# Performance work log

Measured on AMD Instinct MI355X. Metric: run time of the kernel, lower is better.

## Reference

```python
import jax, jax.numpy as jnp
import numpy as np

B, T, DIN, H = 8, 512, 256, 512
D = 2 * H            # d_model = 1024
HEADS, DH, DEPTH, M = 8, 128, 2, 256  # M = nb_features
FF = 4 * D
KEPS = 1e-4          # performer kernel epsilon


def setup_inputs() -> dict:
    key = jax.random.key(0)
    ks = iter(jax.random.split(key, 64))
    def nrm(shape, s=1.0):
        return jax.random.normal(next(ks), shape, jnp.float32) * s
    inp = {"x": nrm((B, T, DIN))}
    # BiLSTM params, stacked over direction [2, ...]; torch gate order i,f,g,o
    for l, din in ((0, DIN), (1, D)):
        s = 1.0 / np.sqrt(H)
        inp[f"l{l}_Wih"] = nrm((2, 4 * H, din), s)
        inp[f"l{l}_Whh"] = nrm((2, 4 * H, H), s)
        inp[f"l{l}_bih"] = nrm((2, 4 * H), s)
        inp[f"l{l}_bhh"] = nrm((2, 4 * H), s)
    # FAVOR+ random projection (buffer), [nb_features, dim_head]
    inp["proj"] = nrm((M, DH))
    sd = 1.0 / np.sqrt(D)
    inp["ln1_g"] = jnp.ones((DEPTH, D)); inp["ln1_b"] = jnp.zeros((DEPTH, D))
    for n in ("Wq", "Wk", "Wv", "Wo"):
        inp[n] = nrm((DEPTH, D, D), sd)
    for n in ("bq", "bk", "bv", "bo"):
        inp[n] = jnp.zeros((DEPTH, D))
    inp["ln2_g"] = jnp.ones((DEPTH, D)); inp["ln2_b"] = jnp.zeros((DEPTH, D))
    inp["Wf1"] = nrm((DEPTH, D, FF), sd); inp["bf1"] = jnp.zeros((DEPTH, FF))
    inp["Wf2"] = nrm((DEPTH, FF, D), 1.0 / np.sqrt(FF)); inp["bf2"] = jnp.zeros((DEPTH, D))
    inp["cW1"] = nrm((D, H), sd); inp["cb1"] = jnp.zeros((H,))
    inp["cW2"] = nrm((H, 2), 1.0 / np.sqrt(H)); inp["cb2"] = jnp.zeros((2,))
    return inp


def _lstm_dir(x, Wih, Whh, bih, bhh, reverse):
    xs = jnp.swapaxes(x, 0, 1)                      # [T,B,Din]
    h0 = jnp.zeros((x.shape[0], H), x.dtype)
    def step(carry, xt):
        h, c = carry
        z = xt @ Wih.T + h @ Whh.T + bih + bhh      # [B,4H]
        i, f, g, o = jnp.split(z, 4, axis=-1)
        c = jax.nn.sigmoid(f) * c + jax.nn.sigmoid(i) * jnp.tanh(g)
        h = jax.nn.sigmoid(o) * jnp.tanh(c)
        return (h, c), h
    _, hs = jax.lax.scan(step, (h0, h0), xs, reverse=reverse)
    return jnp.swapaxes(hs, 0, 1)                   # [B,T,H], time-aligned


def _bilstm(x, Wih, Whh, bih, bhh):
    fwd = _lstm_dir(x, Wih[0], Whh[0], bih[0], bhh[0], False)
    bwd = _lstm_dir(x, Wih[1], Whh[1], bih[1], bhh[1], True)
    return jnp.concatenate([fwd, bwd], axis=-1)     # [B,T,2H]


def _ln(x, g, b):
    mu = jnp.mean(x, -1, keepdims=True)
    v = jnp.mean((x - mu) ** 2, -1, keepdims=True)
    return (x - mu) * jax.lax.rsqrt(v + 1e-5) * g + b


def _favor(data, proj, is_query):
    # softmax_kernel of performer-pytorch (eval mode, fixed projection)
    dn = DH ** -0.25
    dd = jnp.einsum('bhnd,md->bhnm', data * dn, proj)
    diag = jnp.sum(data * data, -1) * (dn * dn * 0.5)      # [b,h,n]
    if is_query:
        mx = jnp.max(dd, axis=-1, keepdims=True)
    else:
        mx = jnp.max(dd, axis=(-1, -2), keepdims=True)
    return (jnp.exp(dd - diag[..., None] - mx) + KEPS) * (M ** -0.5)


def _heads(x, W, b):
    return (x @ W + b).reshape(B, T, HEADS, DH).transpose(0, 2, 1, 3)


def reference(x, l0_Wih, l0_Whh, l0_bih, l0_bhh, l1_Wih, l1_Whh, l1_bih, l1_bhh,
              proj, ln1_g, ln1_b, Wq, bq, Wk, bk, Wv, bv, Wo, bo,
              ln2_g, ln2_b, Wf1, bf1, Wf2, bf2, cW1, cb1, cW2, cb2):
    h = _bilstm(x, l0_Wih, l0_Whh, l0_bih, l0_bhh)
    h = _bilstm(h, l1_Wih, l1_Whh, l1_bih, l1_bhh)          # [B,T,D]
    for i in range(DEPTH):
        # pre-norm FAVOR+ self-attention, non-causal linear attention
        y = _ln(h, ln1_g[i], ln1_b[i])
        q = _favor(_heads(y, Wq[i], bq[i]), proj, True)     # [b,h,n,m]
        k = _favor(_heads(y, Wk[i], bk[i]), proj, False)
        v = _heads(y, Wv[i], bv[i])                         # [b,h,n,d]
        dinv = 1.0 / jnp.einsum('bhnm,bhm->bhn', q, k.sum(axis=2))
        ctx = jnp.einsum('bhnm,bhnd->bhmd', k, v)
        o = jnp.einsum('bhnm,bhmd->bhnd', q, ctx) * dinv[..., None]
        o = o.transpose(0, 2, 1, 3).reshape(B, T, D)
        h = h + (o @ Wo[i] + bo[i])
        # pre-norm feedforward (GELU, mult 4)
        y = _ln(h, ln2_g[i], ln2_b[i])
        h = h + (jax.nn.gelu(y @ Wf1[i] + bf1[i], approximate=False) @ Wf2[i] + bf2[i])
    pooled = h.mean(axis=1)                                 # [B,D]
    logits = jax.nn.relu(pooled @ cW1 + cb1) @ cW2 + cb2    # [B,2]
    return logits
```

## Files before the change

### kernel.cpp

```cpp
#include <hip/hip_runtime.h>

#define KEPS 1e-4f

typedef __attribute__((ext_vector_type(8))) short bf16x8;
typedef __attribute__((ext_vector_type(4))) float f32x4;
typedef __attribute__((ext_vector_type(4))) unsigned u32x4;
typedef unsigned short u16;

__device__ float g_z0[2u*512*2048*8];
__device__ float g_z1[2u*512*2048*8];
__device__ float g_hres[8u*512*1024];
__device__ float g_qlin[8u*8*512*128];
__device__ float g_klin[8u*8*512*128];
__device__ float g_vlin[8u*8*512*128];
__device__ float g_qp[8u*8*512*256];
__device__ float g_ddb[8u*8*512*256];
__device__ float g_kT[8u*8*256*512];
__device__ float g_ctx[64u*256*128];
__device__ float g_bs0[2*2048];
__device__ float g_bs1[2*2048];
__device__ float g_diagq[32768];
__device__ float g_diagk[32768];
__device__ float g_kmx[64];
__device__ float g_ksum[64*256];
__device__ float g_dinv[32768];
__device__ __align__(16) unsigned g_hbuf[2*2*8*256];
__device__ float g_pooled[8*1024];

__device__ u16 g_xbf[8u*512*256];
__device__ u16 g_x1bf[8u*512*1024];
__device__ u16 g_ybf[8u*512*1024];
__device__ u16 g_ylo[8u*512*1024];
__device__ u16 g_obufbf[8u*512*1024];
__device__ u16 g_ffbbf[8u*512*4096];
__device__ u16 g_qhi[8u*8*512*128];
__device__ u16 g_qlo2[8u*8*512*128];
__device__ u16 g_khi[8u*8*512*128];
__device__ u16 g_klo2[8u*8*512*128];
__device__ u16 g_wih0b[2u*2048*256];
__device__ u16 g_wih1b[2u*2048*1024];
__device__ u16 g_wvt[2u*1024*1024];
__device__ u16 g_wot[2u*1024*1024];
__device__ u16 g_wf1t[2u*4096*1024];
__device__ u16 g_wf2t[2u*1024*4096];
__device__ u16 g_wqth[2u*1024*1024];
__device__ u16 g_wqtl[2u*1024*1024];
__device__ u16 g_wkth[2u*1024*1024];
__device__ u16 g_wktl[2u*1024*1024];
__device__ u16 g_projh[256*128];
__device__ u16 g_projl[256*128];

__device__ __forceinline__ float gelu_f(float x) {
  return 0.5f * x * (1.f + erff(x * 0.70710678118654752f));
}
__device__ __forceinline__ unsigned f2bf(float f) {
  unsigned x = __float_as_uint(f);
  return (x + 0x7FFFu + ((x >> 16) & 1u)) >> 16;
}
__device__ __forceinline__ float bf2f(unsigned h) {
  return __uint_as_float(h << 16);
}
__device__ __forceinline__ u32x4 ld16_sc1(const unsigned* p) {
  u32x4 v;
  asm volatile("global_load_dwordx4 %0, %1, off sc1\n\ts_waitcnt vmcnt(0)"
               : "=v"(v) : "v"(p) : "memory");
  return v;
}
__device__ __forceinline__ void st16_sc1(unsigned* p, u32x4 v) {
  asm volatile("global_store_dwordx4 %0, %1, off sc1" :: "v"(p), "v"(v) : "memory");
}
__device__ __forceinline__ void bar_raw() {
  asm volatile("s_waitcnt lgkmcnt(0)" ::: "memory");
  __builtin_amdgcn_sched_barrier(0);
  __builtin_amdgcn_s_barrier();
  __builtin_amdgcn_sched_barrier(0);
}
__device__ __forceinline__ void gll16(const void* g, void* l) {
  __builtin_amdgcn_global_load_lds(
      (const __attribute__((address_space(1))) void*)g,
      (__attribute__((address_space(3))) void*)l, 16, 0, 0);
}

__global__ void k_add2(float* __restrict__ dst, const float* __restrict__ a,
                       const float* __restrict__ b, int n) {
  int i = blockIdx.x * 256 + threadIdx.x;
  if (i < n) dst[i] = a[i] + b[i];
}
__global__ void k_cvt(const float* __restrict__ src, u16* __restrict__ dst, int n4) {
  int i = blockIdx.x * 256 + threadIdx.x;
  if (i < n4) {
    float4 v = ((const float4*)src)[i];
    ushort4 o; o.x=(u16)f2bf(v.x); o.y=(u16)f2bf(v.y); o.z=(u16)f2bf(v.z); o.w=(u16)f2bf(v.w);
    ((ushort4*)dst)[i] = o;
  }
}
__global__ void k_scale_split(const float* __restrict__ a, u16* __restrict__ dh,
                              u16* __restrict__ dl, float s, int n) {
  int i = blockIdx.x*256 + threadIdx.x;
  if (i < n) {
    float v = a[i]*s;
    unsigned h = f2bf(v);
    dh[i] = (u16)h; dl[i] = (u16)f2bf(v - bf2f(h));
  }
}
__global__ void k_w2bfT(const float* __restrict__ src, u16* __restrict__ dst,
                        int K, int N, long long sBS, long long dBS)
{
  __shared__ float tile[32][33];
  const int z = blockIdx.z;
  const int n0 = blockIdx.x*32, k0 = blockIdx.y*32;
  const int tx = threadIdx.x, ty = threadIdx.y;
  const float* s = src + (long long)z*sBS;
  u16* d = dst + (long long)z*dBS;
  #pragma unroll
  for (int j = 0; j < 4; ++j)
    tile[ty + j*8][tx] = s[(long long)(k0 + ty + j*8)*N + n0 + tx];
  __syncthreads();
  #pragma unroll
  for (int j = 0; j < 4; ++j)
    d[(long long)(n0 + ty + j*8)*K + k0 + tx] = (u16)f2bf(tile[tx][ty + j*8]);
}
__global__ void k_w2bfT_split(const float* __restrict__ src, u16* __restrict__ dh,
                              u16* __restrict__ dl, int K, int N,
                              long long sBS, long long dBS)
{
  __shared__ float tile[32][33];
  const int z = blockIdx.z;
  const int n0 = blockIdx.x*32, k0 = blockIdx.y*32;
  const int tx = threadIdx.x, ty = threadIdx.y;
  const float* s = src + (long long)z*sBS;
  #pragma unroll
  for (int j = 0; j < 4; ++j)
    tile[ty + j*8][tx] = s[(long long)(k0 + ty + j*8)*N + n0 + tx];
  __syncthreads();
  #pragma unroll
  for (int j = 0; j < 4; ++j) {
    const float v = tile[tx][ty + j*8];
    const unsigned h = f2bf(v);
    const long long off = (long long)z*dBS + (long long)(n0 + ty + j*8)*K + k0 + tx;
    dh[off] = (u16)h; dl[off] = (u16)f2bf(v - bf2f(h));
  }
}

template<int MODE>
__global__ __launch_bounds__(256)
void k_bgemm(const u16* __restrict__ A, const u16* __restrict__ Bw,
             const float* __restrict__ bias, void* __restrict__ Cv,
             int Ndim, int Kdim,
             long long aBS, long long bBS, long long cBS, long long biasBS)
{
  __shared__ __align__(16) u16 As[128*32];
  __shared__ __align__(16) u16 Bs[128*32];
  const int tid = threadIdx.x;
  const int m0 = blockIdx.y * 128, n0 = blockIdx.x * 128, z = blockIdx.z;
  const u16* Ab = A + (long long)z*aBS;
  const u16* Bb = Bw + (long long)z*bBS;
  const int wv = tid >> 6, l = tid & 63;
  const int wm = wv >> 1, wn = wv & 1;
  const int lr = l & 15, lk = l >> 4;
  const int lrow = l >> 2, lkq = (l & 3)*8;
  f32x4 acc[4][4];
  #pragma unroll
  for (int i=0;i<4;++i)
    #pragma unroll
    for (int j=0;j<4;++j) acc[i][j] = (f32x4){0.f,0.f,0.f,0.f};

  for (int k0 = 0; k0 < Kdim; k0 += 32) {
    #pragma unroll
    for (int q = 0; q < 2; ++q) {
      const int r = wv*32 + q*16 + lrow;
      gll16(&Ab[(long long)(m0 + r)*Kdim + k0 + lkq], &As[(wv*32 + q*16)*32]);
      gll16(&Bb[(long long)(n0 + r)*Kdim + k0 + lkq], &Bs[(wv*32 + q*16)*32]);
    }
    __syncthreads();
    bf16x8 af[4], bfr[4];
    #pragma unroll
    for (int i=0;i<4;++i) af[i]  = *(bf16x8*)&As[(wm*64 + i*16 + lr)*32 + lk*8];
    #pragma unroll
    for (int j=0;j<4;++j) bfr[j] = *(bf16x8*)&Bs[(wn*64 + j*16 + lr)*32 + lk*8];
    #pragma unroll
    for (int i=0;i<4;++i)
      #pragma unroll
      for (int j=0;j<4;++j)
        acc[i][j] = __builtin_amdgcn_mfma_f32_16x16x32_bf16(af[i], bfr[j], acc[i][j], 0, 0, 0);
    __syncthreads();
  }

  #pragma unroll
  for (int j=0;j<4;++j) {
    const int n = n0 + wn*64 + j*16 + lr;
    const float bvv = bias ? bias[(long long)z*biasBS + n] : 0.f;
    #pragma unroll
    for (int i=0;i<4;++i) {
      #pragma unroll
      for (int r=0;r<4;++r) {
        const int m = m0 + wm*64 + i*16 + lk*4 + r;
        float v = acc[i][j][r] + bvv;
        if (MODE == 0) {
          ((float*)Cv)[(long long)z*cBS + (long long)m*Ndim + n] = v;
        } else if (MODE == 1) {
          const int b_ = m >> 9, t_ = m & 511;
          ((float*)Cv)[(long long)z*cBS + ((long long)t_*2048 + n)*8 + b_] = v;
        } else if (MODE == 2) {
          const int b_ = m >> 9, t_ = m & 511;
          const int hd = n >> 7;
          ((float*)Cv)[(((long long)(b_*8 + hd))*512 + t_)*128 + (n & 127)] = v;
        } else if (MODE == 3) {
          float* cp = (float*)Cv + (long long)m*Ndim + n;
          *cp += v;
        } else if (MODE == 4) {
          ((u16*)Cv)[(long long)m*Ndim + n] = (u16)f2bf(gelu_f(v));
        }
      }
    }
  }
}

template<int MODE>
__global__ __launch_bounds__(256)
void k_b3gemm(const u16* __restrict__ Ah, const u16* __restrict__ Al,
              const u16* __restrict__ Bh, const u16* __restrict__ Bl,
              const float* __restrict__ bias, float* __restrict__ Cf,
              u16* __restrict__ Chi, u16* __restrict__ Clo,
              int Ndim, int Kdim)
{
  __shared__ __align__(16) u16 Ash[128*32];
  __shared__ __align__(16) u16 Asl[128*32];
  __shared__ __align__(16) u16 Bsh[128*32];
  __shared__ __align__(16) u16 Bsl[128*32];
  const int tid = threadIdx.x;
  const int m0 = blockIdx.y * 128, n0 = blockIdx.x * 128;
  const int wv = tid >> 6, l = tid & 63;
  const int wm = wv >> 1, wn = wv & 1;
  const int lr = l & 15, lk = l >> 4;
  const int lrow = l >> 2, lkq = (l & 3)*8;
  f32x4 acc[4][4];
  #pragma unroll
  for (int i=0;i<4;++i)
    #pragma unroll
    for (int j=0;j<4;++j) acc[i][j] = (f32x4){0.f,0.f,0.f,0.f};

  for (int k0 = 0; k0 < Kdim; k0 += 32) {
    #pragma unroll
    for (int q = 0; q < 2; ++q) {
      const int r = wv*32 + q*16 + lrow;
      const long long ao = (long long)(m0 + r)*Kdim + k0 + lkq;
      const long long bo = (long long)(n0 + r)*Kdim + k0 + lkq;
      const int lb = (wv*32 + q*16)*32;
      gll16(&Ah[ao], &Ash[lb]);
      gll16(&Al[ao], &Asl[lb]);
      gll16(&Bh[bo], &Bsh[lb]);
      gll16(&Bl[bo], &Bsl[lb]);
    }
    __syncthreads();
    bf16x8 ah[4], al_[4], bh[4], bl_[4];
    #pragma unroll
    for (int i=0;i<4;++i) {
      ah[i]  = *(bf16x8*)&Ash[(wm*64 + i*16 + lr)*32 + lk*8];
      al_[i] = *(bf16x8*)&Asl[(wm*64 + i*16 + lr)*32 + lk*8];
    }
    #pragma unroll
    for (int j=0;j<4;++j) {
      bh[j]  = *(bf16x8*)&Bsh[(wn*64 + j*16 + lr)*32 + lk*8];
      bl_[j] = *(bf16x8*)&Bsl[(wn*64 + j*16 + lr)*32 + lk*8];
    }
    #pragma unroll
    for (int i=0;i<4;++i)
      #pragma unroll
      for (int j=0;j<4;++j) {
        acc[i][j] = __builtin_amdgcn_mfma_f32_16x16x32_bf16(ah[i],  bh[j],  acc[i][j], 0, 0, 0);
        acc[i][j] = __builtin_amdgcn_mfma_f32_16x16x32_bf16(ah[i],  bl_[j], acc[i][j], 0, 0, 0);
        acc[i][j] = __builtin_amdgcn_mfma_f32_16x16x32_bf16(al_[i], bh[j],  acc[i][j], 0, 0, 0);
      }
    __syncthreads();
  }

  #pragma unroll
  for (int j=0;j<4;++j) {
    const int n = n0 + wn*64 + j*16 + lr;
    const float bvv = bias ? bias[n] : 0.f;
    #pragma unroll
    for (int i=0;i<4;++i) {
      #pragma unroll
      for (int r=0;r<4;++r) {
        const int m = m0 + wm*64 + i*16 + lk*4 + r;
        float v = acc[i][j][r] + bvv;
        if (MODE == 0) {
          Cf[(long long)m*Ndim + n] = v;
        } else if (MODE == 2) {
          const int b_ = m >> 9, t_ = m & 511;
          const int hd = n >> 7;
          const long long off = (((long long)(b_*8 + hd))*512 + t_)*128 + (n & 127);
          Cf[off] = v;
          const unsigned h = f2bf(v);
          Chi[off] = (u16)h;
          Clo[off] = (u16)f2bf(v - bf2f(h));
        }
      }
    }
  }
}

template<int BT, int MODE>
__global__ __launch_bounds__(256)
void k_gemm(const float* __restrict__ A, const float* __restrict__ Bw,
            const float* __restrict__ bias, float* __restrict__ C,
            int Mdim, int Ndim, int Kdim,
            long long aBS, long long bBS, long long cBS, long long biasBS,
            const float* __restrict__ aux)
{
  __shared__ float As[16][128];
  __shared__ float Bs[16][128];
  const int tid = threadIdx.x;
  const int tx = tid & 15, ty = tid >> 4;
  const int m0 = blockIdx.y * 128, n0 = blockIdx.x * 128;
  const int z = blockIdx.z;
  const float* Ab = A + (long long)z * aBS;
  const float* Bb = Bw + (long long)z * bBS;
  float acc[8][8] = {};

  for (int k0 = 0; k0 < Kdim; k0 += 16) {
    #pragma unroll
    for (int l0 = 0; l0 < 512; l0 += 256) {
      const int ll = l0 + tid;
      const int r = ll >> 2, kq = (ll & 3) * 4;
      float4 v = *(const float4*)&Ab[(long long)(m0 + r) * Kdim + k0 + kq];
      As[kq+0][r] = v.x; As[kq+1][r] = v.y; As[kq+2][r] = v.z; As[kq+3][r] = v.w;
    }
    if (BT) {
      #pragma unroll
      for (int l0 = 0; l0 < 512; l0 += 256) {
        const int ll = l0 + tid;
        const int r = ll >> 2, kq = (ll & 3) * 4;
        float4 v = *(const float4*)&Bb[(long long)(n0 + r) * Kdim + k0 + kq];
        Bs[kq+0][r] = v.x; Bs[kq+1][r] = v.y; Bs[kq+2][r] = v.z; Bs[kq+3][r] = v.w;
      }
    } else {
      #pragma unroll
      for (int l0 = 0; l0 < 512; l0 += 256) {
        const int ll = l0 + tid;
        const int kr = ll >> 5, n4 = (ll & 31) * 4;
        *(float4*)&Bs[kr][n4] = *(const float4*)&Bb[(long long)(k0 + kr) * Ndim + n0 + n4];
      }
    }
    __syncthreads();
    #pragma unroll
    for (int kk = 0; kk < 16; ++kk) {
      float4 af0 = *(const float4*)&As[kk][ty*4];
      float4 af1 = *(const float4*)&As[kk][64 + ty*4];
      float4 bf0 = *(const float4*)&Bs[kk][tx*4];
      float4 bf1 = *(const float4*)&Bs[kk][64 + tx*4];
      float av[8] = {af0.x,af0.y,af0.z,af0.w,af1.x,af1.y,af1.z,af1.w};
      float bv[8] = {bf0.x,bf0.y,bf0.z,bf0.w,bf1.x,bf1.y,bf1.z,bf1.w};
      #pragma unroll
      for (int i = 0; i < 8; ++i)
        #pragma unroll
        for (int j = 0; j < 8; ++j)
          acc[i][j] = fmaf(av[i], bv[j], acc[i][j]);
    }
    __syncthreads();
  }

  float* Cz = C + (long long)z * cBS;
  #pragma unroll
  for (int i = 0; i < 8; ++i) {
    const int m = m0 + ((i < 4) ? (ty*4 + i) : (64 + ty*4 + (i - 4)));
    #pragma unroll
    for (int jb = 0; jb < 2; ++jb) {
      const int ci = n0 + (jb ? 64 : 0) + tx*4;
      float4 v;
      v.x = acc[i][jb*4+0]; v.y = acc[i][jb*4+1];
      v.z = acc[i][jb*4+2]; v.w = acc[i][jb*4+3];
      if (MODE == 0) {
        *(float4*)&Cz[(long long)m * Ndim + ci] = v;
      } else if (MODE == 5) {
        const int b_ = z >> 3, hd = z & 7;
        const float sc = aux[(long long)z*512 + m];
        u16* Cb = (u16*)C;
        const long long off = ((long long)(b_*512 + m))*1024 + hd*128 + ci;
        Cb[off+0] = (u16)f2bf(v.x*sc);
        Cb[off+1] = (u16)f2bf(v.y*sc);
        Cb[off+2] = (u16)f2bf(v.z*sc);
        Cb[off+3] = (u16)f2bf(v.w*sc);
      }
    }
  }
}

template<int OBF>
__global__ __launch_bounds__(512)
void k_lstm7(const float* __restrict__ Z, const float* __restrict__ Whh,
             float* __restrict__ outf, u16* __restrict__ outb,
             unsigned* __restrict__ hbufU)
{
  extern __shared__ char smem[];
  short*  Wl    = (short*)smem;
  short*  hl    = (short*)(smem + 131072);
  float*  gates = (float*)(smem + 139264);

  const int slice = blockIdx.x & 15, dir = blockIdx.x >> 4;
  const int tid = threadIdx.x;
  const int u0 = slice * 32;

  for (int blk = tid; blk < 8192; blk += 512) {
    const int lr2 = blk >> 6, bi = blk & 63;
    const long long src = ((long long)dir*2048 + (lr2>>5)*512 + u0 + (lr2&31))*512 + bi*8;
    float4 w0 = *(const float4*)&Whh[src];
    float4 w1 = *(const float4*)&Whh[src + 4];
    unsigned* dst = (unsigned*)&Wl[lr2*512 + (((bi + lr2) & 63) << 3)];
    dst[0] = f2bf(w0.x) | (f2bf(w0.y) << 16);
    dst[1] = f2bf(w0.z) | (f2bf(w0.w) << 16);
    dst[2] = f2bf(w1.x) | (f2bf(w1.y) << 16);
    dst[3] = f2bf(w1.z) | (f2bf(w1.w) << 16);
  }
  for (int i = tid; i < 2048; i += 512) ((unsigned*)hl)[i] = 0u;

  const int wv = tid >> 6, l = tid & 63;
  const int arow = wv*16 + (l & 15);
  const int bb   = l & 7;
  const int qoff = l >> 4;
  const int jj = tid >> 3, bcomb = tid & 7;
  float cst = 0.f;
  int gt = 1;
  int pt = 2;

  for (int s = 0; s < 512; ++s) {
    const int t = dir ? (511 - s) : s;
    float z0v = 0.f, z1v = 0.f, z2v = 0.f, z3v = 0.f;
    if (tid < 256) {
      const float* zp = Z + (((long long)dir*512 + t)*16384) + (u0 + jj)*8 + bcomb;
      z0v = zp[0]; z1v = zp[4096]; z2v = zp[8192]; z3v = zp[12288];
    }
    if (s > 0) {
      const unsigned base = ((unsigned)((s & 1)*2 + dir)) * 2048;
      const unsigned* src = &hbufU[base + tid*4];
      u32x4 v;
      for (;;) {
        v = ld16_sc1(src);
        const int tag = (int)((v.x & 1u) | (((v.x >> 16) & 1u) << 1) | ((v.y & 1u) << 2));
        if (tag == gt) break;
      }
      const int b = tid >> 6, q = tid & 63;
      *(u32x4*)((char*)hl + b*1024 + (((q + b) & 63) << 4)) = v;
    }
    bar_raw();
    f32x4 acc0 = {0.f,0.f,0.f,0.f}, acc1 = {0.f,0.f,0.f,0.f};
    #pragma unroll
    for (int ks = 0; ks < 8; ++ks) {
      const int qa = (2*ks)*4 + qoff, qb = (2*ks + 1)*4 + qoff;
      bf16x8 a0 = *(bf16x8*)&Wl[arow*512 + (((qa + arow) & 63) << 3)];
      bf16x8 b0 = *(bf16x8*)&hl[bb*512   + (((qa + bb)   & 63) << 3)];
      acc0 = __builtin_amdgcn_mfma_f32_16x16x32_bf16(a0, b0, acc0, 0, 0, 0);
      bf16x8 a1 = *(bf16x8*)&Wl[arow*512 + (((qb + arow) & 63) << 3)];
      bf16x8 b1 = *(bf16x8*)&hl[bb*512   + (((qb + bb)   & 63) << 3)];
      acc1 = __builtin_amdgcn_mfma_f32_16x16x32_bf16(a1, b1, acc1, 0, 0, 0);
    }
    const int bcol = l & 15;
    if (bcol < 8) {
      #pragma unroll
      for (int r = 0; r < 4; ++r)
        gates[(wv*16 + qoff*4 + r)*8 + bcol] = acc0[r] + acc1[r];
    }
    bar_raw();
    if (tid < 256) {
      const float gi = gates[jj*8        + bcomb] + z0v;
      const float gf = gates[(32+jj)*8   + bcomb] + z1v;
      const float gg = gates[(64+jj)*8   + bcomb] + z2v;
      const float go = gates[(96+jj)*8   + bcomb] + z3v;
      const float ig = 1.f/(1.f + expf(-gi));
      const float fg = 1.f/(1.f + expf(-gf));
      const float og = 1.f/(1.f + expf(-go));
      cst = fg*cst + ig*tanhf(gg);
      const float hv = og*tanhf(cst);
      const unsigned hb = f2bf(hv);
      if (OBF) outb[((long long)(bcomb*512 + t))*1024 + (dir<<9) + u0 + jj] = (u16)hb;
      else     outf[((long long)(bcomb*512 + t))*1024 + (dir<<9) + u0 + jj] = hv;
      unsigned p  = hb | (((unsigned)__shfl_down((int)hb, 8, 64)) << 16);
      unsigned y1 = (unsigned)__shfl_down((int)p, 16, 64);
      unsigned y2 = (unsigned)__shfl_down((int)p, 32, 64);
      unsigned y3 = (unsigned)__shfl_down((int)p, 48, 64);
      if (s != 511 && (l & 56) == 0) {
        u32x4 w;
        w.x = (p  & ~0x00010001u) | (unsigned)(pt & 1) | (((unsigned)(pt >> 1) & 1u) << 16);
        w.y = (y1 & ~1u) | ((unsigned)(pt >> 2) & 1u);
        w.z = y2; w.w = y3;
        const unsigned base2 = ((unsigned)(((s+1) & 1)*2 + dir)) * 2048;
        st16_sc1(&hbufU[base2 + bcomb*256 + (u0 >> 1) + wv*4], w);
      }
    }
    gt = (gt == 7) ? 1 : gt + 1;
    pt = (pt == 7) ? 1 : pt + 1;
  }
}

__global__ __launch_bounds__(256)
void k_ln(const float* __restrict__ X, const float* __restrict__ gw,
          const float* __restrict__ bw, u16* __restrict__ Yh, u16* __restrict__ Yl)
{
  const int row = blockIdx.x, tid = threadIdx.x;
  const float* xr = X + (long long)row * 1024;
  float4 v = *(const float4*)&xr[tid*4];
  float s  = v.x + v.y + v.z + v.w;
  float ss = v.x*v.x + v.y*v.y + v.z*v.z + v.w*v.w;
  #pragma unroll
  for (int off = 1; off < 64; off <<= 1) {
    s  += __shfl_xor(s, off, 64);
    ss += __shfl_xor(ss, off, 64);
  }
  __shared__ float rs[4], rss[4];
  const int w = tid >> 6;
  if ((tid & 63) == 0) { rs[w] = s; rss[w] = ss; }
  __syncthreads();
  s  = rs[0] + rs[1] + rs[2] + rs[3];
  ss = rss[0] + rss[1] + rss[2] + rss[3];
  const float mu = s * (1.f/1024.f);
  const float var = ss * (1.f/1024.f) - mu*mu;
  const float rstd = rsqrtf(var + 1e-5f);
  float4 g4 = *(const float4*)&gw[tid*4];
  float4 b4 = *(const float4*)&bw[tid*4];
  float4 o;
  o.x = (v.x - mu)*rstd*g4.x + b4.x;
  o.y = (v.y - mu)*rstd*g4.y + b4.y;
  o.z = (v.z - mu)*rstd*g4.z + b4.z;
  o.w = (v.w - mu)*rstd*g4.w + b4.w;
  ushort4 hh, ll;
  hh.x=(u16)f2bf(o.x); ll.x=(u16)f2bf(o.x - bf2f(f2bf(o.x)));
  hh.y=(u16)f2bf(o.y); ll.y=(u16)f2bf(o.y - bf2f(f2bf(o.y)));
  hh.z=(u16)f2bf(o.z); ll.z=(u16)f2bf(o.z - bf2f(f2bf(o.z)));
  hh.w=(u16)f2bf(o.w); ll.w=(u16)f2bf(o.w - bf2f(f2bf(o.w)));
  *(ushort4*)&Yh[(long long)row*1024 + tid*4] = hh;
  *(ushort4*)&Yl[(long long)row*1024 + tid*4] = ll;
}

__global__ void k_diag(const float* __restrict__ X, float* __restrict__ dout)
{
  const int tid = threadIdx.x;
  const int row = blockIdx.x*4 + (tid >> 6);
  const int lane = tid & 63;
  float2 v = *(const float2*)&X[(long long)row*128 + lane*2];
  float ss = v.x*v.x + v.y*v.y;
  #pragma unroll
  for (int off = 1; off < 64; off <<= 1) ss += __shfl_xor(ss, off, 64);
  if (lane == 0) dout[row] = ss * 0.044194173824159216f;
}

__global__ void k_favq(float* __restrict__ dd, const float* __restrict__ diag)
{
  const int tid = threadIdx.x;
  const int row = blockIdx.x*4 + (tid >> 6);
  const int lane = tid & 63;
  float4 v = *(const float4*)&dd[(long long)row*256 + lane*4];
  float mx = fmaxf(fmaxf(v.x, v.y), fmaxf(v.z, v.w));
  #pragma unroll
  for (int off = 1; off < 64; off <<= 1) mx = fmaxf(mx, __shfl_xor(mx, off, 64));
  const float dg = diag[row];
  float4 o;
  o.x = (expf(v.x - dg - mx) + KEPS)*0.0625f;
  o.y = (expf(v.y - dg - mx) + KEPS)*0.0625f;
  o.z = (expf(v.z - dg - mx) + KEPS)*0.0625f;
  o.w = (expf(v.w - dg - mx) + KEPS)*0.0625f;
  *(float4*)&dd[(long long)row*256 + lane*4] = o;
}

__global__ __launch_bounds__(256)
void k_kmax(const float* __restrict__ dd, float* __restrict__ kmx)
{
  const int bh = blockIdx.x, tid = threadIdx.x;
  const float* p = dd + (long long)bh * 131072;
  float mx = -3.4e38f;
  for (int i = tid*4; i < 131072; i += 1024) {
    float4 v = *(const float4*)&p[i];
    mx = fmaxf(mx, fmaxf(fmaxf(v.x, v.y), fmaxf(v.z, v.w)));
  }
  #pragma unroll
  for (int off = 1; off < 64; off <<= 1) mx = fmaxf(mx, __shfl_xor(mx, off, 64));
  __shared__ float red[4];
  if ((tid & 63) == 0) red[tid >> 6] = mx;
  __syncthreads();
  if (tid == 0) kmx[bh] = fmaxf(fmaxf(red[0], red[1]), fmaxf(red[2], red[3]));
}

__global__ void k_fkT(const float* __restrict__ dd, const float* __restrict__ diag,
                      const float* __restrict__ kmx, float* __restrict__ kT)
{
  __shared__ float tile[32][33];
  const int bh = blockIdx.z;
  const int t0 = blockIdx.x * 32, m0 = blockIdx.y * 32;
  const int tx = threadIdx.x, ty = threadIdx.y;
  const float km = kmx[bh];
  #pragma unroll
  for (int j = 0; j < 4; ++j) {
    const int t = t0 + ty + j*8;
    const float v = dd[((long long)bh*512 + t)*256 + m0 + tx];
    tile[ty + j*8][tx] = (expf(v - diag[bh*512 + t] - km) + KEPS) * 0.0625f;
  }
  __syncthreads();
  #pragma unroll
  for (int j = 0; j < 4; ++j) {
    const int m = m0 + ty + j*8;
    kT[((long long)bh*256 + m)*512 + t0 + tx] = tile[tx][ty + j*8];
  }
}

__global__ void k_ksum(const float* __restrict__ kT, float* __restrict__ ksum)
{
  const int tid = threadIdx.x;
  const int row = blockIdx.x*4 + (tid >> 6);
  const int lane = tid & 63;
  float4 a = *(const float4*)&kT[(long long)row*512 + lane*8];
  float4 b = *(const float4*)&kT[(long long)row*512 + lane*8 + 4];
  float s = a.x+a.y+a.z+a.w + b.x+b.y+b.z+b.w;
  #pragma unroll
  for (int off = 1; off < 64; off <<= 1) s += __shfl_xor(s, off, 64);
  if (lane == 0) ksum[row] = s;
}

__global__ void k_dinv(const float* __restrict__ qp, const float* __restrict__ ksum,
                       float* __restrict__ dinv)
{
  const int tid = threadIdx.x;
  const int row = blockIdx.x*4 + (tid >> 6);
  const int lane = tid & 63;
  const int bh = row >> 9;
  float4 q = *(const float4*)&qp[(long long)row*256 + lane*4];
  float4 k = *(const float4*)&ksum[bh*256 + lane*4];
  float s = q.x*k.x + q.y*k.y + q.z*k.z + q.w*k.w;
  #pragma unroll
  for (int off = 1; off < 64; off <<= 1) s += __shfl_xor(s, off, 64);
  if (lane == 0) dinv[row] = 1.f / s;
}

__global__ void k_pool(const float* __restrict__ h, float* __restrict__ pooled)
{
  const int idx = blockIdx.x * 256 + threadIdx.x;
  const int b = idx >> 10, d = idx & 1023;
  const float* p = h + (long long)b * 524288 + d;
  float s0=0,s1=0,s2=0,s3=0;
  for (int t0 = 0; t0 < 512; t0 += 4) {
    s0 += p[(long long)(t0+0)*1024];
    s1 += p[(long long)(t0+1)*1024];
    s2 += p[(long long)(t0+2)*1024];
    s3 += p[(long long)(t0+3)*1024];
  }
  pooled[idx] = (s0+s1+s2+s3) * (1.f/512.f);
}

__global__ __launch_bounds__(256)
void k_cls(const float* __restrict__ pooled, const float* __restrict__ W1,
           const float* __restrict__ b1, const float* __restrict__ W2,
           const float* __restrict__ b2, float* __restrict__ out)
{
  const int b = blockIdx.x, tid = threadIdx.x;
  __shared__ float pl[1024];
  __shared__ float hd[512];
  *(float4*)&pl[tid*4] = *(const float4*)&pooled[b*1024 + tid*4];
  __syncthreads();
  for (int u = tid; u < 512; u += 256) {
    float acc = b1[u];
    for (int k = 0; k < 1024; ++k) acc = fmaf(pl[k], W1[(long long)k*512 + u], acc);
    hd[u] = fmaxf(acc, 0.f);
  }
  __syncthreads();
  if (tid < 2) {
    float acc = b2[tid];
    for (int k = 0; k < 512; ++k) acc = fmaf(hd[k], W2[k*2 + tid], acc);
    out[b*2 + tid] = acc;
  }
}

static void* symp(const void* s) { void* p = nullptr; (void)hipGetSymbolAddress(&p, s); return p; }

extern "C" void kernel_launch(void* const* d_in, const int* in_sizes, int n_in,
                              void* d_out, int out_size, void* d_ws, size_t ws_size,
                              hipStream_t stream)
{
  (void)in_sizes; (void)n_in; (void)d_ws; (void)ws_size; (void)out_size;
  const float* x     = (const float*)d_in[0];
  const float* l0Wih = (const float*)d_in[1];
  const float* l0Whh = (const float*)d_in[2];
  const float* l0bih = (const float*)d_in[3];
  const float* l0bhh = (const float*)d_in[4];
  const float* l1Wih = (const float*)d_in[5];
  const float* l1Whh = (const float*)d_in[6];
  const float* l1bih = (const float*)d_in[7];
  const float* l1bhh = (const float*)d_in[8];
  const float* proj  = (const float*)d_in[9];
  const float* ln1g  = (const float*)d_in[10];
  const float* ln1b  = (const float*)d_in[11];
  const float* Wq    = (const float*)d_in[12];
  const float* Wk    = (const float*)d_in[13];
  const float* Wv    = (const float*)d_in[14];
  const float* Wo    = (const float*)d_in[15];
  const float* bq    = (const float*)d_in[16];
  const float* bk    = (const float*)d_in[17];
  const float* bv    = (const float*)d_in[18];
  const float* bo    = (const float*)d_in[19];
  const float* ln2g  = (const float*)d_in[20];
  const float* ln2b  = (const float*)d_in[21];
  const float* Wf1   = (const float*)d_in[22];
  const float* bf1   = (const float*)d_in[23];
  const float* Wf2   = (const float*)d_in[24];
  const float* bf2   = (const float*)d_in[25];
  const float* cW1   = (const float*)d_in[26];
  const float* cb1   = (const float*)d_in[27];
  const float* cW2   = (const float*)d_in[28];
  const float* cb2   = (const float*)d_in[29];

  float* z0    = (float*)symp(HIP_SYMBOL(g_z0));
  float* z1    = (float*)symp(HIP_SYMBOL(g_z1));
  float* hres  = (float*)symp(HIP_SYMBOL(g_hres));
  float* qlin  = (float*)symp(HIP_SYMBOL(g_qlin));
  float* klin  = (float*)symp(HIP_SYMBOL(g_klin));
  float* vlin  = (float*)symp(HIP_SYMBOL(g_vlin));
  float* qp    = (float*)symp(HIP_SYMBOL(g_qp));
  float* ddb   = (float*)symp(HIP_SYMBOL(g_ddb));
  float* kT    = (float*)symp(HIP_SYMBOL(g_kT));
  float* ctx   = (float*)symp(HIP_SYMBOL(g_ctx));
  float* bs0   = (float*)symp(HIP_SYMBOL(g_bs0));
  float* bs1   = (float*)symp(HIP_SYMBOL(g_bs1));
  float* diagq = (float*)symp(HIP_SYMBOL(g_diagq));
  float* diagk = (float*)symp(HIP_SYMBOL(g_diagk));
  float* kmx   = (float*)symp(HIP_SYMBOL(g_kmx));
  float* ksum  = (float*)symp(HIP_SYMBOL(g_ksum));
  float* dinv  = (float*)symp(HIP_SYMBOL(g_dinv));
  unsigned* hbuf = (unsigned*)symp(HIP_SYMBOL(g_hbuf));
  float* pooled= (float*)symp(HIP_SYMBOL(g_pooled));
  u16* xbf   = (u16*)symp(HIP_SYMBOL(g_xbf));
  u16* x1bf  = (u16*)symp(HIP_SYMBOL(g_x1bf));
  u16* ybf   = (u16*)symp(HIP_SYMBOL(g_ybf));
  u16* ylo   = (u16*)symp(HIP_SYMBOL(g_ylo));
  u16* obufbf= (u16*)symp(HIP_SYMBOL(g_obufbf));
  u16* ffbbf = (u16*)symp(HIP_SYMBOL(g_ffbbf));
  u16* qhi   = (u16*)symp(HIP_SYMBOL(g_qhi));
  u16* qlo2  = (u16*)symp(HIP_SYMBOL(g_qlo2));
  u16* khi   = (u16*)symp(HIP_SYMBOL(g_khi));
  u16* klo2  = (u16*)symp(HIP_SYMBOL(g_klo2));
  u16* wih0b = (u16*)symp(HIP_SYMBOL(g_wih0b));
  u16* wih1b = (u16*)symp(HIP_SYMBOL(g_wih1b));
  u16* wvt   = (u16*)symp(HIP_SYMBOL(g_wvt));
  u16* wot   = (u16*)symp(HIP_SYMBOL(g_wot));
  u16* wf1t  = (u16*)symp(HIP_SYMBOL(g_wf1t));
  u16* wf2t  = (u16*)symp(HIP_SYMBOL(g_wf2t));
  u16* wqth  = (u16*)symp(HIP_SYMBOL(g_wqth));
  u16* wqtl  = (u16*)symp(HIP_SYMBOL(g_wqtl));
  u16* wkth  = (u16*)symp(HIP_SYMBOL(g_wkth));
  u16* wktl  = (u16*)symp(HIP_SYMBOL(g_wktl));
  u16* projh = (u16*)symp(HIP_SYMBOL(g_projh));
  u16* projl = (u16*)symp(HIP_SYMBOL(g_projl));

  const float dn = 0.29730177875068026f;
  const int LSTM_LDS = 143360;
  (void)hipFuncSetAttribute((const void*)k_lstm7<1>,
                            hipFuncAttributeMaxDynamicSharedMemorySize, LSTM_LDS);
  (void)hipFuncSetAttribute((const void*)k_lstm7<0>,
                            hipFuncAttributeMaxDynamicSharedMemorySize, LSTM_LDS);

  k_add2<<<16, 256, 0, stream>>>(bs0, l0bih, l0bhh, 4096);
  k_add2<<<16, 256, 0, stream>>>(bs1, l1bih, l1bhh, 4096);
  k_scale_split<<<128, 256, 0, stream>>>(proj, projh, projl, dn, 32768);

  k_cvt<<<1024, 256, 0, stream>>>(x, xbf, 262144);
  k_cvt<<<1024, 256, 0, stream>>>(l0Wih, wih0b, 262144);
  k_cvt<<<4096, 256, 0, stream>>>(l1Wih, wih1b, 1048576);
  k_w2bfT<<<dim3(32,32,2),  dim3(32,8), 0, stream>>>(Wv,  wvt,  1024, 1024, 1048576LL, 1048576LL);
  k_w2bfT<<<dim3(32,32,2),  dim3(32,8), 0, stream>>>(Wo,  wot,  1024, 1024, 1048576LL, 1048576LL);
  k_w2bfT<<<dim3(128,32,2), dim3(32,8), 0, stream>>>(Wf1, wf1t, 1024, 4096, 4194304LL, 4194304LL);
  k_w2bfT<<<dim3(32,128,2), dim3(32,8), 0, stream>>>(Wf2, wf2t, 4096, 1024, 4194304LL, 4194304LL);
  k_w2bfT_split<<<dim3(32,32,2), dim3(32,8), 0, stream>>>(Wq, wqth, wqtl, 1024, 1024, 1048576LL, 1048576LL);
  k_w2bfT_split<<<dim3(32,32,2), dim3(32,8), 0, stream>>>(Wk, wkth, wktl, 1024, 1024, 1048576LL, 1048576LL);

  k_bgemm<1><<<dim3(16,32,2), 256, 0, stream>>>(xbf, wih0b, bs0, z0,
      2048, 256, 0LL, 524288LL, 8388608LL, 2048LL);
  k_lstm7<1><<<32, 512, LSTM_LDS, stream>>>(z0, l0Whh, nullptr, x1bf, hbuf);
  k_bgemm<1><<<dim3(16,32,2), 256, 0, stream>>>(x1bf, wih1b, bs1, z1,
      2048, 1024, 0LL, 2097152LL, 8388608LL, 2048LL);
  k_lstm7<0><<<32, 512, LSTM_LDS, stream>>>(z1, l1Whh, hres, nullptr, hbuf);

  for (int i = 0; i < 2; ++i) {
    const long long wOffU = (long long)i * 1048576;
    k_ln<<<4096, 256, 0, stream>>>(hres, ln1g + i*1024, ln1b + i*1024, ybf, ylo);
    k_b3gemm<2><<<dim3(8,32,1), 256, 0, stream>>>(ybf, ylo, wqth + wOffU, wqtl + wOffU,
        bq + i*1024, qlin, qhi, qlo2, 1024, 1024);
    k_b3gemm<2><<<dim3(8,32,1), 256, 0, stream>>>(ybf, ylo, wkth + wOffU, wktl + wOffU,
        bk + i*1024, klin, khi, klo2, 1024, 1024);
    k_bgemm<2><<<dim3(8,32,1), 256, 0, stream>>>(ybf, wvt + wOffU, bv + i*1024, vlin,
        1024, 1024, 0LL, 0LL, 0LL, 0LL);
    k_diag<<<8192, 256, 0, stream>>>(qlin, diagq);
    k_diag<<<8192, 256, 0, stream>>>(klin, diagk);
    k_b3gemm<0><<<dim3(2,256,1), 256, 0, stream>>>(qhi, qlo2, projh, projl,
        nullptr, qp, nullptr, nullptr, 256, 128);
    k_favq<<<8192, 256, 0, stream>>>(qp, diagq);
    k_b3gemm<0><<<dim3(2,256,1), 256, 0, stream>>>(khi, klo2, projh, projl,
        nullptr, ddb, nullptr, nullptr, 256, 128);
    k_kmax<<<64, 256, 0, stream>>>(ddb, kmx);
    k_fkT<<<dim3(16,8,64), dim3(32,8), 0, stream>>>(ddb, diagk, kmx, kT);
    k_ksum<<<4096, 256, 0, stream>>>(kT, ksum);
    k_gemm<0,0><<<dim3(1,2,64), 256, 0, stream>>>(kT, vlin, nullptr, ctx,
        256, 128, 512, 131072LL, 65536LL, 32768LL, 0LL, nullptr);
    k_dinv<<<8192, 256, 0, stream>>>(qp, ksum, dinv);
    k_gemm<0,5><<<dim3(1,4,64), 256, 0, stream>>>(qp, ctx, nullptr, (float*)obufbf,
        512, 128, 256, 131072LL, 32768LL, 0LL, 0LL, dinv);
    k_bgemm<3><<<dim3(8,32,1), 256, 0, stream>>>(obufbf, wot + wOffU, bo + i*1024, hres,
        1024, 1024, 0LL, 0LL, 0LL, 0LL);
    k_ln<<<4096, 256, 0, stream>>>(hres, ln2g + i*1024, ln2b + i*1024, ybf, ylo);
    k_bgemm<4><<<dim3(32,32,1), 256, 0, stream>>>(ybf, wf1t + (long long)i*4194304,
        bf1 + i*4096, ffbbf, 4096, 1024, 0LL, 0LL, 0LL, 0LL);
    k_bgemm<3><<<dim3(8,32,1), 256, 0, stream>>>(ffbbf, wf2t + (long long)i*4194304,
        bf2 + i*1024, hres, 1024, 4096, 0LL, 0LL, 0LL, 0LL);
  }

  k_pool<<<32, 256, 0, stream>>>(hres, pooled);
  k_cls<<<8, 256, 0, stream>>>(pooled, cW1, cb1, cW2, cb2, (float*)d_out);
}
```

Measured before the change: 5.284 ms.

## Pin LSTM blocks to one XCD, stage h via LDS, fuse q diag into favq

The LSTM recurrence kernel is launched with 8x the blocks, and all but every eighth exit immediately. Assuming round-robin block placement across XCDs, the 32 working blocks should then share one XCD and its L2, which would make the per-step hidden-state exchange through global memory cheaper. Hidden outputs are now gathered in LDS and written by 32 threads instead of being packed with wave shuffles, at the cost of one more block barrier per timestep. Separately, the query diagonal term is computed inside k_favq, which removes one kernel launch and its intermediate buffer.

After: 5.034 ms. 4.7% less time.

```diff
diff --git a/kernel.cpp b/kernel.cpp
--- a/kernel.cpp
+++ b/kernel.cpp
@@ -19,7 +19,6 @@
 __device__ float g_ctx[64u*256*128];
 __device__ float g_bs0[2*2048];
 __device__ float g_bs1[2*2048];
-__device__ float g_diagq[32768];
 __device__ float g_diagk[32768];
 __device__ float g_kmx[64];
 __device__ float g_ksum[64*256];
@@ -69,12 +68,6 @@
 __device__ __forceinline__ void st16_sc1(unsigned* p, u32x4 v) {
   asm volatile("global_store_dwordx4 %0, %1, off sc1" :: "v"(p), "v"(v) : "memory");
 }
-__device__ __forceinline__ void bar_raw() {
-  asm volatile("s_waitcnt lgkmcnt(0)" ::: "memory");
-  __builtin_amdgcn_sched_barrier(0);
-  __builtin_amdgcn_s_barrier();
-  __builtin_amdgcn_sched_barrier(0);
-}
 __device__ __forceinline__ void gll16(const void* g, void* l) {
   __builtin_amdgcn_global_load_lds(
       (const __attribute__((address_space(1))) void*)g,
@@ -389,16 +382,19 @@
 
 template<int OBF>
 __global__ __launch_bounds__(512)
-void k_lstm7(const float* __restrict__ Z, const float* __restrict__ Whh,
+void k_lstm8(const float* __restrict__ Z, const float* __restrict__ Whh,
              float* __restrict__ outf, u16* __restrict__ outb,
              unsigned* __restrict__ hbufU)
 {
+  if ((blockIdx.x & 7) != 0) return;
   extern __shared__ char smem[];
-  short*  Wl    = (short*)smem;
-  short*  hl    = (short*)(smem + 131072);
-  float*  gates = (float*)(smem + 139264);
-
-  const int slice = blockIdx.x & 15, dir = blockIdx.x >> 4;
+  short*          Wl    = (short*)smem;
+  short*          hl    = (short*)(smem + 131072);
+  float*          gates = (float*)(smem + 139264);
+  unsigned short* houts = (unsigned short*)(smem + 143360);
+
+  const int wg = blockIdx.x >> 3;
+  const int slice = wg & 15, dir = wg >> 4;
   const int tid = threadIdx.x;
   const int u0 = slice * 32;
 
@@ -443,7 +439,7 @@
       const int b = tid >> 6, q = tid & 63;
       *(u32x4*)((char*)hl + b*1024 + (((q + b) & 63) << 4)) = v;
     }
-    bar_raw();
+    __syncthreads();
     f32x4 acc0 = {0.f,0.f,0.f,0.f}, acc1 = {0.f,0.f,0.f,0.f};
     #pragma unroll
     for (int ks = 0; ks < 8; ++ks) {
@@ -461,7 +457,7 @@
       for (int r = 0; r < 4; ++r)
         gates[(wv*16 + qoff*4 + r)*8 + bcol] = acc0[r] + acc1[r];
     }
-    bar_raw();
+    __syncthreads();
     if (tid < 256) {
       const float gi = gates[jj*8        + bcomb] + z0v;
       const float gf = gates[(32+jj)*8   + bcomb] + z1v;
@@ -475,18 +471,16 @@
       const unsigned hb = f2bf(hv);
       if (OBF) outb[((long long)(bcomb*512 + t))*1024 + (dir<<9) + u0 + jj] = (u16)hb;
       else     outf[((long long)(bcomb*512 + t))*1024 + (dir<<9) + u0 + jj] = hv;
-      unsigned p  = hb | (((unsigned)__shfl_down((int)hb, 8, 64)) << 16);
-      unsigned y1 = (unsigned)__shfl_down((int)p, 16, 64);
-      unsigned y2 = (unsigned)__shfl_down((int)p, 32, 64);
-      unsigned y3 = (unsigned)__shfl_down((int)p, 48, 64);
-      if (s != 511 && (l & 56) == 0) {
-        u32x4 w;
-        w.x = (p  & ~0x00010001u) | (unsigned)(pt & 1) | (((unsigned)(pt >> 1) & 1u) << 16);
-        w.y = (y1 & ~1u) | ((unsigned)(pt >> 2) & 1u);
-        w.z = y2; w.w = y3;
-        const unsigned base2 = ((unsigned)(((s+1) & 1)*2 + dir)) * 2048;
-        st16_sc1(&hbufU[base2 + bcomb*256 + (u0 >> 1) + wv*4], w);
-      }
+      houts[bcomb*32 + jj] = (unsigned short)hb;
+    }
+    __syncthreads();
+    if (s != 511 && tid < 32) {
+      const int b = tid >> 2, q4 = tid & 3;
+      u32x4 w = *(const u32x4*)&houts[b*32 + q4*8];
+      w.x = (w.x & ~0x00010001u) | (unsigned)(pt & 1) | (((unsigned)(pt >> 1) & 1u) << 16);
+      w.y = (w.y & ~1u) | ((unsigned)(pt >> 2) & 1u);
+      const unsigned base2 = ((unsigned)(((s+1) & 1)*2 + dir)) * 2048;
+      st16_sc1(&hbufU[base2 + b*256 + (u0 >> 1) + q4*4], w);
     }
     gt = (gt == 7) ? 1 : gt + 1;
     pt = (pt == 7) ? 1 : pt + 1;
@@ -544,16 +538,21 @@
   if (lane == 0) dout[row] = ss * 0.044194173824159216f;
 }
 
-__global__ void k_favq(float* __restrict__ dd, const float* __restrict__ diag)
+__global__ void k_favq(float* __restrict__ dd, const float* __restrict__ qlin)
 {
   const int tid = threadIdx.x;
   const int row = blockIdx.x*4 + (tid >> 6);
   const int lane = tid & 63;
   float4 v = *(const float4*)&dd[(long long)row*256 + lane*4];
+  float2 qv = *(const float2*)&qlin[(long long)row*128 + lane*2];
   float mx = fmaxf(fmaxf(v.x, v.y), fmaxf(v.z, v.w));
-  #pragma unroll
-  for (int off = 1; off < 64; off <<= 1) mx = fmaxf(mx, __shfl_xor(mx, off, 64));
-  const float dg = diag[row];
+  float ss = qv.x*qv.x + qv.y*qv.y;
+  #pragma unroll
+  for (int off = 1; off < 64; off <<= 1) {
+    mx = fmaxf(mx, __shfl_xor(mx, off, 64));
+    ss += __shfl_xor(ss, off, 64);
+  }
+  const float dg = ss * 0.044194173824159216f;
   float4 o;
   o.x = (expf(v.x - dg - mx) + KEPS)*0.0625f;
   o.y = (expf(v.y - dg - mx) + KEPS)*0.0625f;
@@ -718,7 +717,6 @@
   float* ctx   = (float*)symp(HIP_SYMBOL(g_ctx));
   float* bs0   = (float*)symp(HIP_SYMBOL(g_bs0));
   float* bs1   = (float*)symp(HIP_SYMBOL(g_bs1));
-  float* diagq = (float*)symp(HIP_SYMBOL(g_diagq));
   float* diagk = (float*)symp(HIP_SYMBOL(g_diagk));
   float* kmx   = (float*)symp(HIP_SYMBOL(g_kmx));
   float* ksum  = (float*)symp(HIP_SYMBOL(g_ksum));
@@ -749,10 +747,10 @@
   u16* projl = (u16*)symp(HIP_SYMBOL(g_projl));
 
   const float dn = 0.29730177875068026f;
-  const int LSTM_LDS = 143360;
-  (void)hipFuncSetAttribute((const void*)k_lstm7<1>,
+  const int LSTM_LDS = 143872;
+  (void)hipFuncSetAttribute((const void*)k_lstm8<1>,
                             hipFuncAttributeMaxDynamicSharedMemorySize, LSTM_LDS);
-  (void)hipFuncSetAttribute((const void*)k_lstm7<0>,
+  (void)hipFuncSetAttribute((const void*)k_lstm8<0>,
                             hipFuncAttributeMaxDynamicSharedMemorySize, LSTM_LDS);
 
   k_add2<<<16, 256, 0, stream>>>(bs0, l0bih, l0bhh, 4096);
@@ -771,10 +769,10 @@
 
   k_bgemm<1><<<dim3(16,32,2), 256, 0, stream>>>(xbf, wih0b, bs0, z0,
       2048, 256, 0LL, 524288LL, 8388608LL, 2048LL);
-  k_lstm7<1><<<32, 512, LSTM_LDS, stream>>>(z0, l0Whh, nullptr, x1bf, hbuf);
+  k_lstm8<1><<<256, 512, LSTM_LDS, stream>>>(z0, l0Whh, nullptr, x1bf, hbuf);
   k_bgemm<1><<<dim3(16,32,2), 256, 0, stream>>>(x1bf, wih1b, bs1, z1,
       2048, 1024, 0LL, 2097152LL, 8388608LL, 2048LL);
-  k_lstm7<0><<<32, 512, LSTM_LDS, stream>>>(z1, l1Whh, hres, nullptr, hbuf);
+  k_lstm8<0><<<256, 512, LSTM_LDS, stream>>>(z1, l1Whh, hres, nullptr, hbuf);
 
   for (int i = 0; i < 2; ++i) {
     const long long wOffU = (long long)i * 1048576;
@@ -785,11 +783,10 @@
         bk + i*1024, klin, khi, klo2, 1024, 1024);
     k_bgemm<2><<<dim3(8,32,1), 256, 0, stream>>>(ybf, wvt + wOffU, bv + i*1024, vlin,
         1024, 1024, 0LL, 0LL, 0LL, 0LL);
-    k_diag<<<8192, 256, 0, stream>>>(qlin, diagq);
     k_diag<<<8192, 256, 0, stream>>>(klin, diagk);
     k_b3gemm<0><<<dim3(2,256,1), 256, 0, stream>>>(qhi, qlo2, projh, projl,
         nullptr, qp, nullptr, nullptr, 256, 128);
-    k_favq<<<8192, 256, 0, stream>>>(qp, diagq);
+    k_favq<<<8192, 256, 0, stream>>>(qp, qlin);
     k_b3gemm<0><<<dim3(2,256,1), 256, 0, stream>>>(khi, klo2, projh, projl,
         nullptr, ddb, nullptr, nullptr, 256, 128);
     k_kmax<<<64, 256, 0, stream>>>(ddb, kmx);
```
